# Kernel optimization log

Measured on AMD Instinct MI355X. Metric: run time of the kernel, lower is better.

Reference implementation:

```python
import jax, jax.numpy as jnp
import numpy as np

TEXT_DIM, GIN = 5000, 128
B, N, E = 4096, 200000, 6400000
AE_HID, AE_EMB, G_HID, G_EMB = 8, 4, 8, 4


def _gcn(x, W, b, src, dst):
    N_ = x.shape[0]
    h = x @ W
    loop = jnp.arange(N_)
    s = jnp.concatenate([src, loop])
    d = jnp.concatenate([dst, loop])
    deg = jax.ops.segment_sum(jnp.ones(s.shape[0], h.dtype), d, num_segments=N_)
    dinv = jnp.where(deg > 0, jax.lax.rsqrt(jnp.maximum(deg, 1e-12)), 0.0)
    norm = dinv[s] * dinv[d]
    out = jax.ops.segment_sum(h[s] * norm[:, None], d, num_segments=N_)
    return out + b


def setup_inputs() -> dict:
    key = jax.random.key(0)
    ks = jax.random.split(key, 20)
    def lin(k, fan_in, fan_out):
        lim = 1.0 / np.sqrt(fan_in)
        kw, kb = jax.random.split(k)
        W = jax.random.uniform(kw, (fan_in, fan_out), jnp.float32, -lim, lim)
        b = jax.random.uniform(kb, (fan_out,), jnp.float32, -lim, lim)
        return W, b
    W_e1, b_e1 = lin(ks[0], TEXT_DIM, AE_HID)
    W_e2, b_e2 = lin(ks[1], AE_HID, AE_EMB)
    W_d1, b_d1 = lin(ks[2], AE_EMB, AE_HID)
    W_d2, b_d2 = lin(ks[3], AE_HID, TEXT_DIM)
    W_g1, b_g1 = lin(ks[4], GIN, G_HID)
    W_g2, b_g2 = lin(ks[5], G_HID, G_EMB)
    W_c, b_c = lin(ks[6], AE_EMB + G_EMB, 1)
    text_x = jax.random.normal(ks[7], (B, TEXT_DIM), jnp.float32)
    node_x = jax.random.normal(ks[8], (N, GIN), jnp.float32)
    edge_index = jax.random.randint(ks[9], (2, E), 0, N, jnp.int64 if jax.config.jax_enable_x64 else jnp.int32)
    batch = jnp.sort(jax.random.randint(ks[10], (N,), 0, B, edge_index.dtype))
    return {"text_x": text_x, "node_x": node_x, "edge_index": edge_index, "batch": batch,
            "W_e1": W_e1, "b_e1": b_e1, "W_e2": W_e2, "b_e2": b_e2,
            "W_d1": W_d1, "b_d1": b_d1, "W_d2": W_d2, "b_d2": b_d2,
            "W_g1": W_g1, "b_g1": b_g1, "W_g2": W_g2, "b_g2": b_g2,
            "W_c": W_c, "b_c": b_c}


def reference(text_x, node_x, edge_index, batch,
              W_e1, b_e1, W_e2, b_e2, W_d1, b_d1, W_d2, b_d2,
              W_g1, b_g1, W_g2, b_g2, W_c, b_c):
    # Autoencoder (eval mode: dropout = identity)
    z_text = jax.nn.relu(jax.nn.relu(text_x @ W_e1 + b_e1) @ W_e2 + b_e2)
    x_hat = jax.nn.sigmoid(jax.nn.relu(z_text @ W_d1 + b_d1) @ W_d2 + b_d2)
    # GNN encoder
    src, dst = edge_index[0], edge_index[1]
    h = jax.nn.relu(_gcn(node_x, W_g1, b_g1, src, dst))
    h = _gcn(h, W_g2, b_g2, src, dst)
    # global mean pool over graphs
    nb = text_x.shape[0]
    sums = jax.ops.segment_sum(h, batch, num_segments=nb)
    cnt = jax.ops.segment_sum(jnp.ones(h.shape[0], h.dtype), batch, num_segments=nb)
    z_graph = sums / jnp.maximum(cnt, 1.0)[:, None]
    z = jnp.concatenate([z_text, z_graph], axis=1)
    logits = z @ W_c + b_c
    return (x_hat, logits, z)
```

## Files before the change

### kernel.cpp

```cpp
#include <hip/hip_runtime.h>

#define BB 4096
#define TD 5000
#define NN 200000
#define EE 6400000
#define NBK 782
#define WS_NEED 40081932ull

__global__ void k_init(const int* __restrict__ e, unsigned int* __restrict__ deg,
                       int* __restrict__ flag) {
    int i = blockIdx.x * 256 + threadIdx.x;
    if (i < NN) deg[i] = 1u;
    if (blockIdx.x == 0) {
        __shared__ int r[256];
        int tid = threadIdx.x;
        int acc = 0;
        for (int k = tid; k < 4096; k += 256) acc |= e[2 * k + 1];
        r[tid] = acc;
        __syncthreads();
        for (int s = 128; s > 0; s >>= 1) {
            if (tid < s) r[tid] |= r[tid + s];
            __syncthreads();
        }
        if (tid == 0) *flag = (r[0] == 0) ? 1 : 0;
    }
}

__device__ void role_rank(int rid, int tid, const int* __restrict__ edge,
                          const int* __restrict__ flag, unsigned int* __restrict__ deg,
                          unsigned int* __restrict__ rnk) {
    int f = *flag;
    int base = rid * 2048 + tid;
    int d[8];
#pragma unroll
    for (int k = 0; k < 8; k++) {
        int e = base + k * 256;
        d[k] = f ? edge[2 * (EE + e)] : edge[EE + e];
    }
    unsigned int rr[8];
#pragma unroll
    for (int k = 0; k < 8; k++) rr[k] = atomicAdd(&deg[d[k]], 1u);
#pragma unroll
    for (int k = 0; k < 8; k++) rnk[base + k * 256] = rr[k];
}

__device__ void role_enc(int row, int tid, const float* __restrict__ text,
                         const float* __restrict__ We1, const float* __restrict__ be1,
                         const float* __restrict__ We2, const float* __restrict__ be2,
                         float* __restrict__ z_text) {
    __shared__ float red[8][256];
    __shared__ float t1[8];
    const float4* xrow = (const float4*)(text + (size_t)row * TD);
    float acc[8];
#pragma unroll
    for (int j = 0; j < 8; j++) acc[j] = 0.f;
    for (int v = tid; v < 1250; v += 256) {
        float4 xv = xrow[v];
        const float4* w = (const float4*)(We1 + (size_t)v * 32);
        float xc[4] = {xv.x, xv.y, xv.z, xv.w};
#pragma unroll
        for (int c = 0; c < 4; c++) {
            float4 wa = w[c * 2], wb = w[c * 2 + 1];
            acc[0] += xc[c] * wa.x; acc[1] += xc[c] * wa.y;
            acc[2] += xc[c] * wa.z; acc[3] += xc[c] * wa.w;
            acc[4] += xc[c] * wb.x; acc[5] += xc[c] * wb.y;
            acc[6] += xc[c] * wb.z; acc[7] += xc[c] * wb.w;
        }
    }
#pragma unroll
    for (int j = 0; j < 8; j++) red[j][tid] = acc[j];
    __syncthreads();
    for (int s = 128; s > 0; s >>= 1) {
        if (tid < s) {
#pragma unroll
            for (int j = 0; j < 8; j++) red[j][tid] += red[j][tid + s];
        }
        __syncthreads();
    }
    if (tid < 8) t1[tid] = fmaxf(red[tid][0] + be1[tid], 0.f);
    __syncthreads();
    if (tid < 4) {
        float z = be2[tid];
#pragma unroll
        for (int k = 0; k < 8; k++) z += t1[k] * We2[k * 4 + tid];
        z_text[row * 4 + tid] = fmaxf(z, 0.f);
    }
}

__device__ void role_mm(int mid, int tid, const float* __restrict__ nodex,
                        const float* __restrict__ Wg1, const float* __restrict__ dinv,
                        float* __restrict__ h0g) {
    __shared__ float W[1024];
    for (int i = tid; i < 1024; i += 256) W[i] = Wg1[i];
    __syncthreads();
    int row = mid * 256 + tid;
    if (row >= NN) return;
    const float4* xr = (const float4*)(nodex + (size_t)row * 128);
    float acc[8];
#pragma unroll
    for (int j = 0; j < 8; j++) acc[j] = 0.f;
#pragma unroll 8
    for (int c = 0; c < 32; c++) {
        float4 v = xr[c];
        const float* wr = &W[c * 32];
#pragma unroll
        for (int j = 0; j < 8; j++)
            acc[j] += v.x * wr[j] + v.y * wr[8 + j] + v.z * wr[16 + j] + v.w * wr[24 + j];
    }
    float di = dinv[row];
    float* o = h0g + (size_t)row * 8;
#pragma unroll
    for (int j = 0; j < 8; j++) o[j] = di * acc[j];
}

__device__ void role_place(int pid, int tid, const int* __restrict__ edge,
                           const int* __restrict__ flag, const unsigned int* __restrict__ indptr,
                           const unsigned int* __restrict__ rnk, int* __restrict__ csr) {
    int f = *flag;
    int base = pid * 1024 + tid;
    int s[4], d[4];
#pragma unroll
    for (int k = 0; k < 4; k++) {
        int e = base + k * 256;
        s[k] = f ? edge[2 * e] : edge[e];
        d[k] = f ? edge[2 * (EE + e)] : edge[EE + e];
    }
    unsigned int rr[4];
#pragma unroll
    for (int k = 0; k < 4; k++) rr[k] = rnk[base + k * 256];
    unsigned int ip[4];
#pragma unroll
    for (int k = 0; k < 4; k++) ip[k] = indptr[d[k]];
#pragma unroll
    for (int k = 0; k < 4; k++) csr[ip[k] + rr[k] - 1u] = s[k];
}

__device__ void role_decode(int row, int tid, const float* __restrict__ zsrc, int zstride,
                            const float* __restrict__ Wd1, const float* __restrict__ bd1,
                            const float* __restrict__ Wd2, const float* __restrict__ bd2,
                            float* __restrict__ xhat) {
    float zz[4];
#pragma unroll
    for (int j = 0; j < 4; j++) zz[j] = zsrc[row * zstride + j];
    float t[8];
#pragma unroll
    for (int k = 0; k < 8; k++) {
        float s = bd1[k];
#pragma unroll
        for (int j = 0; j < 4; j++) s += zz[j] * Wd1[j * 8 + k];
        t[k] = fmaxf(s, 0.f);
    }
    float4* orow = (float4*)(xhat + (size_t)row * TD);
    for (int c4 = tid; c4 < 1250; c4 += 256) {
        float4 s = *(const float4*)(bd2 + c4 * 4);
#pragma unroll
        for (int k = 0; k < 8; k++) {
            float4 w = *(const float4*)(Wd2 + (size_t)k * TD + c4 * 4);
            s.x += t[k] * w.x; s.y += t[k] * w.y;
            s.z += t[k] * w.z; s.w += t[k] * w.w;
        }
        s.x = 1.f / (1.f + expf(-s.x));
        s.y = 1.f / (1.f + expf(-s.y));
        s.z = 1.f / (1.f + expf(-s.z));
        s.w = 1.f / (1.f + expf(-s.w));
        orow[c4] = s;
    }
}

__device__ void role_g1(int gid, int tid, const unsigned int* __restrict__ indptr,
                        const int* __restrict__ csr, const float* __restrict__ h0g,
                        const float* __restrict__ dinv, const float* __restrict__ bg1,
                        const float* __restrict__ Wg2, float* __restrict__ h2g) {
    __shared__ float W[32];
    __shared__ float b1[8];
    __shared__ float h1s[4][8];
    if (tid < 32) W[tid] = Wg2[tid];
    if (tid < 8) b1[tid] = bg1[tid];
    __syncthreads();
    int wid = tid >> 6, lane = tid & 63;
    int i = gid * 4 + wid;
    if (i < NN) {
        int beg = indptr[i], end = indptr[i + 1];
        int f = lane & 7;
        float a = 0.f;
        for (int k = beg + (lane >> 3); k < end; k += 8)
            a += h0g[(size_t)csr[k] * 8 + f];
        a += __shfl_xor(a, 8, 64);
        a += __shfl_xor(a, 16, 64);
        a += __shfl_xor(a, 32, 64);
        if (lane < 8) {
            float di = dinv[i];
            h1s[wid][f] = fmaxf(di * (a + h0g[(size_t)i * 8 + f]) + b1[f], 0.f);
        }
    }
    __syncthreads();
    if (i < NN && lane < 4) {
        float di = dinv[i];
        float s = 0.f;
#pragma unroll
        for (int k = 0; k < 8; k++) s += h1s[wid][k] * W[k * 4 + lane];
        h2g[(size_t)i * 4 + lane] = di * s;
    }
}

__global__ __launch_bounds__(256) void k_fat1(
    const int* __restrict__ edge, const int* __restrict__ flag,
    unsigned int* __restrict__ deg, unsigned int* __restrict__ rnk,
    const float* __restrict__ text,
    const float* __restrict__ We1, const float* __restrict__ be1,
    const float* __restrict__ We2, const float* __restrict__ be2,
    float* __restrict__ z_text)
{
    int bid = blockIdx.x, tid = threadIdx.x;
    if (bid < 6250) {
        if (bid & 1) role_enc(bid >> 1, tid, text, We1, be1, We2, be2, z_text);
        else role_rank(bid >> 1, tid, edge, flag, deg, rnk);
    } else {
        role_enc(3125 + (bid - 6250), tid, text, We1, be1, We2, be2, z_text);
    }
}

__global__ __launch_bounds__(256) void k_fat2(
    const int* __restrict__ edge, const int* __restrict__ flag,
    const unsigned int* __restrict__ indptr, const unsigned int* __restrict__ rnk,
    int* __restrict__ csr, const float* __restrict__ nodex,
    const float* __restrict__ Wg1, const float* __restrict__ dinv,
    float* __restrict__ h0g)
{
    int bid = blockIdx.x, tid = threadIdx.x;
    if (bid < 6250) role_place(bid, tid, edge, flag, indptr, rnk, csr);
    else role_mm(bid - 6250, tid, nodex, Wg1, dinv, h0g);
}

__global__ __launch_bounds__(256) void k_g1(
    const unsigned int* __restrict__ indptr, const int* __restrict__ csr,
    const float* __restrict__ h0g, const float* __restrict__ dinv,
    const float* __restrict__ bg1, const float* __restrict__ Wg2,
    float* __restrict__ h2g)
{
    role_g1(blockIdx.x, threadIdx.x, indptr, csr, h0g, dinv, bg1, Wg2, h2g);
}

__global__ __launch_bounds__(256) void k_g1_ws(
    const unsigned int* __restrict__ indptr, const int* __restrict__ csr,
    const float* __restrict__ h0g, const float* __restrict__ dinv,
    const float* __restrict__ bg1, const float* __restrict__ Wg2,
    float* __restrict__ h2g,
    const float* __restrict__ z_text,
    const float* __restrict__ Wd1, const float* __restrict__ bd1,
    const float* __restrict__ Wd2, const float* __restrict__ bd2,
    float* __restrict__ xhat)
{
    int bid = blockIdx.x, tid = threadIdx.x;
    if (bid < 8192) {
        if (bid & 1) role_decode(bid >> 1, tid, z_text, 4, Wd1, bd1, Wd2, bd2, xhat);
        else role_g1(bid >> 1, tid, indptr, csr, h0g, dinv, bg1, Wg2, h2g);
    } else {
        role_g1(bid - 4096, tid, indptr, csr, h0g, dinv, bg1, Wg2, h2g);
    }
}

__global__ __launch_bounds__(256) void k_dec(
    const float* __restrict__ zsrc,
    const float* __restrict__ Wd1, const float* __restrict__ bd1,
    const float* __restrict__ Wd2, const float* __restrict__ bd2,
    float* __restrict__ xhat)
{
    role_decode(blockIdx.x, threadIdx.x, zsrc, 8, Wd1, bd1, Wd2, bd2, xhat);
}

__global__ void kA_all(const unsigned int* __restrict__ deg, float* __restrict__ dinv,
                       unsigned int* __restrict__ bsum, const int* __restrict__ batch,
                       const int* __restrict__ flag, unsigned int* __restrict__ bnd) {
    __shared__ unsigned int s[256];
    int tid = threadIdx.x;
    int i = blockIdx.x * 256 + tid;
    unsigned int c = 0u;
    if (i < NN) {
        unsigned int u = deg[i];
        dinv[i] = rsqrtf((float)u);
        c = u - 1u;
        int fg = *flag;
        int b = fg ? batch[2 * i] : batch[i];
        int bp = (i == 0) ? -1 : (fg ? batch[2 * (i - 1)] : batch[i - 1]);
        for (int bb = bp + 1; bb <= b; bb++) bnd[bb] = (unsigned int)i;
        if (i == NN - 1)
            for (int bb = b + 1; bb <= BB; bb++) bnd[bb] = (unsigned int)NN;
    }
    s[tid] = c;
    __syncthreads();
    for (int st = 128; st > 0; st >>= 1) {
        if (tid < st) s[tid] += s[tid + st];
        __syncthreads();
    }
    if (tid == 0) bsum[blockIdx.x] = s[0];
}

__global__ void kB_scanblocks(const unsigned int* __restrict__ bsum, unsigned int* __restrict__ bpre,
                              unsigned int* __restrict__ indptr) {
    __shared__ unsigned int s[1024];
    int t = threadIdx.x;
    s[t] = (t < NBK) ? bsum[t] : 0u;
    __syncthreads();
    for (int off = 1; off < 1024; off <<= 1) {
        unsigned int v = (t >= off) ? s[t - off] : 0u;
        __syncthreads();
        s[t] += v;
        __syncthreads();
    }
    if (t < NBK) bpre[t] = (t == 0) ? 0u : s[t - 1];
    if (t == 0) indptr[NN] = EE;
}

__global__ void kC_indptr(const unsigned int* __restrict__ deg, const unsigned int* __restrict__ bpre,
                          unsigned int* __restrict__ indptr) {
    __shared__ unsigned int s[256];
    int tid = threadIdx.x;
    int i = blockIdx.x * 256 + tid;
    unsigned int c = (i < NN) ? (deg[i] - 1u) : 0u;
    s[tid] = c;
    __syncthreads();
    for (int off = 1; off < 256; off <<= 1) {
        unsigned int v = (tid >= off) ? s[tid - off] : 0u;
        __syncthreads();
        s[tid] += v;
        __syncthreads();
    }
    if (i < NN) indptr[i] = bpre[blockIdx.x] + s[tid] - c;
}

__global__ __launch_bounds__(256) void k_gather2(
    const unsigned int* __restrict__ indptr, const int* __restrict__ csr_src,
    const float* __restrict__ h2g, const float* __restrict__ dinv,
    const float* __restrict__ bg2, float* __restrict__ h2f)
{
    __shared__ float b2[4];
    int tid = threadIdx.x;
    if (tid < 4) b2[tid] = bg2[tid];
    __syncthreads();
    int wid = tid >> 6, lane = tid & 63;
    int i = blockIdx.x * 4 + wid;
    if (i >= NN) return;
    int beg = indptr[i], end = indptr[i + 1];
    int f = lane & 3;
    float a = 0.f;
    for (int k = beg + (lane >> 2); k < end; k += 16)
        a += h2g[(size_t)csr_src[k] * 4 + f];
    a += __shfl_xor(a, 4, 64);
    a += __shfl_xor(a, 8, 64);
    a += __shfl_xor(a, 16, 64);
    a += __shfl_xor(a, 32, 64);
    if (lane < 4) {
        float di = dinv[i];
        h2f[(size_t)i * 4 + f] = di * (a + h2g[(size_t)i * 4 + f]) + b2[f];
    }
}

__global__ __launch_bounds__(256) void k_final(
    const float* __restrict__ h2f, const unsigned int* __restrict__ bnd,
    const float* __restrict__ z_text, const float* __restrict__ Wc,
    const float* __restrict__ bc, float* __restrict__ out_logits,
    float* __restrict__ out_z)
{
    __shared__ float red[256][4];
    int g = blockIdx.x, tid = threadIdx.x;
    int lo = bnd[g], hi = bnd[g + 1];
    float a0 = 0.f, a1 = 0.f, a2 = 0.f, a3 = 0.f;
    for (int i = lo + tid; i < hi; i += 256) {
        float4 v = *(const float4*)(h2f + (size_t)i * 4);
        a0 += v.x; a1 += v.y; a2 += v.z; a3 += v.w;
    }
    red[tid][0] = a0; red[tid][1] = a1; red[tid][2] = a2; red[tid][3] = a3;
    __syncthreads();
    for (int s = 128; s > 0; s >>= 1) {
        if (tid < s) {
            red[tid][0] += red[tid + s][0]; red[tid][1] += red[tid + s][1];
            red[tid][2] += red[tid + s][2]; red[tid][3] += red[tid + s][3];
        }
        __syncthreads();
    }
    if (tid == 0) {
        float c = (float)(hi - lo);
        c = fmaxf(c, 1.f);
        float z8[8];
#pragma unroll
        for (int j = 0; j < 4; j++) z8[j] = z_text[g * 4 + j];
#pragma unroll
        for (int j = 0; j < 4; j++) z8[4 + j] = red[0][j] / c;
        float l = bc[0];
#pragma unroll
        for (int k = 0; k < 8; k++) l += z8[k] * Wc[k];
        out_logits[g] = l;
#pragma unroll
        for (int k = 0; k < 8; k++) out_z[g * 8 + k] = z8[k];
    }
}

extern "C" void kernel_launch(void* const* d_in, const int* in_sizes, int n_in,
                              void* d_out, int out_size, void* d_ws, size_t ws_size,
                              hipStream_t stream) {
    const float* text  = (const float*)d_in[0];
    const float* nodex = (const float*)d_in[1];
    const int* edge    = (const int*)d_in[2];
    const int* batch   = (const int*)d_in[3];
    const float* We1 = (const float*)d_in[4];
    const float* be1 = (const float*)d_in[5];
    const float* We2 = (const float*)d_in[6];
    const float* be2 = (const float*)d_in[7];
    const float* Wd1 = (const float*)d_in[8];
    const float* bd1 = (const float*)d_in[9];
    const float* Wd2 = (const float*)d_in[10];
    const float* bd2 = (const float*)d_in[11];
    const float* Wg1 = (const float*)d_in[12];
    const float* bg1 = (const float*)d_in[13];
    const float* Wg2 = (const float*)d_in[14];
    const float* bg2 = (const float*)d_in[15];
    const float* Wc  = (const float*)d_in[16];
    const float* bc  = (const float*)d_in[17];

    float* out_xhat   = (float*)d_out;
    float* out_logits = out_xhat + (size_t)BB * TD;
    float* out_z      = out_logits + BB;

    const bool use_ws = (ws_size >= WS_NEED);

    float *h0g, *h2g, *h2f, *dinv, *z_text;
    unsigned int *deg, *indptr, *rnk, *bsum, *bpre, *bnd;
    int *csr, *flag;

    if (use_ws) {
        char* w = (char*)d_ws;
        h0g    = (float*)(w + 0);
        h2g    = (float*)(w + 6400000);
        h2f    = (float*)(w + 9600000);
        dinv   = (float*)(w + 12800000);
        indptr = (unsigned int*)(w + 13600000);
        csr    = (int*)(w + 14400004);
        z_text = (float*)(w + 40000004);
        bnd    = (unsigned int*)(w + 40065540);
        flag   = (int*)(w + 40081928);
        char* o = (char*)d_out;
        rnk  = (unsigned int*)(o + 0);
        deg  = (unsigned int*)(o + 25600000);
        bsum = (unsigned int*)(o + 26400000);
        bpre = (unsigned int*)(o + 26403128);
    } else {
        char* o = (char*)d_out;
        h0g    = (float*)(o + 0);
        h2g    = (float*)(o + 6400000);
        h2f    = (float*)(o + 9600000);
        dinv   = (float*)(o + 12800000);
        deg    = (unsigned int*)(o + 13600000);
        indptr = (unsigned int*)(o + 14400000);
        rnk    = (unsigned int*)(o + 15200004);
        csr    = (int*)(o + 40800004);
        bsum   = (unsigned int*)(o + 66400004);
        bpre   = (unsigned int*)(o + 66403132);
        z_text = (float*)(o + 66406260);
        bnd    = (unsigned int*)(o + 66471796);
        flag   = (int*)(o + 66488184);
    }

    k_init<<<NBK, 256, 0, stream>>>(edge, deg, flag);
    k_fat1<<<7221, 256, 0, stream>>>(edge, flag, deg, rnk,
                                     text, We1, be1, We2, be2, z_text);
    kA_all<<<NBK, 256, 0, stream>>>(deg, dinv, bsum, batch, flag, bnd);
    kB_scanblocks<<<1, 1024, 0, stream>>>(bsum, bpre, indptr);
    kC_indptr<<<NBK, 256, 0, stream>>>(deg, bpre, indptr);
    k_fat2<<<7032, 256, 0, stream>>>(edge, flag, indptr, rnk, csr,
                                     nodex, Wg1, dinv, h0g);

    if (use_ws) {
        k_g1_ws<<<54096, 256, 0, stream>>>(indptr, csr, h0g, dinv, bg1, Wg2, h2g,
                                           z_text, Wd1, bd1, Wd2, bd2, out_xhat);
    } else {
        k_g1<<<(NN + 3) / 4, 256, 0, stream>>>(indptr, csr, h0g, dinv, bg1, Wg2, h2g);
    }

    k_gather2<<<(NN + 3) / 4, 256, 0, stream>>>(indptr, csr, h2g, dinv, bg2, h2f);
    k_final<<<BB, 256, 0, stream>>>(h2f, bnd, z_text, Wc, bc, out_logits, out_z);

    if (!use_ws) {
        k_dec<<<BB, 256, 0, stream>>>(out_z, Wd1, bd1, Wd2, bd2, out_xhat);
    }
}
```

Baseline: 729.8 us.

## Pack rank with destination, fuse node matmul into degree kernel, shrink workspace

```diff
diff --git a/kernel.cpp b/kernel.cpp
--- a/kernel.cpp
+++ b/kernel.cpp
@@ -5,7 +5,7 @@
 #define NN 200000
 #define EE 6400000
 #define NBK 782
-#define WS_NEED 40081932ull
+#define WS_NEED 36881932ull
 
 __global__ void k_init(const int* __restrict__ e, unsigned int* __restrict__ deg,
                        int* __restrict__ flag) {
@@ -28,7 +28,7 @@
 
 __device__ void role_rank(int rid, int tid, const int* __restrict__ edge,
                           const int* __restrict__ flag, unsigned int* __restrict__ deg,
-                          unsigned int* __restrict__ rnk) {
+                          unsigned int* __restrict__ rnkpack) {
     int f = *flag;
     int base = rid * 2048 + tid;
     int d[8];
@@ -41,7 +41,7 @@
 #pragma unroll
     for (int k = 0; k < 8; k++) rr[k] = atomicAdd(&deg[d[k]], 1u);
 #pragma unroll
-    for (int k = 0; k < 8; k++) rnk[base + k * 256] = rr[k];
+    for (int k = 0; k < 8; k++) rnkpack[base + k * 256] = (rr[k] << 18) | (unsigned int)d[k];
 }
 
 __device__ void role_enc(int row, int tid, const float* __restrict__ text,
@@ -85,54 +85,6 @@
         for (int k = 0; k < 8; k++) z += t1[k] * We2[k * 4 + tid];
         z_text[row * 4 + tid] = fmaxf(z, 0.f);
     }
-}
-
-__device__ void role_mm(int mid, int tid, const float* __restrict__ nodex,
-                        const float* __restrict__ Wg1, const float* __restrict__ dinv,
-                        float* __restrict__ h0g) {
-    __shared__ float W[1024];
-    for (int i = tid; i < 1024; i += 256) W[i] = Wg1[i];
-    __syncthreads();
-    int row = mid * 256 + tid;
-    if (row >= NN) return;
-    const float4* xr = (const float4*)(nodex + (size_t)row * 128);
-    float acc[8];
-#pragma unroll
-    for (int j = 0; j < 8; j++) acc[j] = 0.f;
-#pragma unroll 8
-    for (int c = 0; c < 32; c++) {
-        float4 v = xr[c];
-        const float* wr = &W[c * 32];
-#pragma unroll
-        for (int j = 0; j < 8; j++)
-            acc[j] += v.x * wr[j] + v.y * wr[8 + j] + v.z * wr[16 + j] + v.w * wr[24 + j];
-    }
-    float di = dinv[row];
-    float* o = h0g + (size_t)row * 8;
-#pragma unroll
-    for (int j = 0; j < 8; j++) o[j] = di * acc[j];
-}
-
-__device__ void role_place(int pid, int tid, const int* __restrict__ edge,
-                           const int* __restrict__ flag, const unsigned int* __restrict__ indptr,
-                           const unsigned int* __restrict__ rnk, int* __restrict__ csr) {
-    int f = *flag;
-    int base = pid * 1024 + tid;
-    int s[4], d[4];
-#pragma unroll
-    for (int k = 0; k < 4; k++) {
-        int e = base + k * 256;
-        s[k] = f ? edge[2 * e] : edge[e];
-        d[k] = f ? edge[2 * (EE + e)] : edge[EE + e];
-    }
-    unsigned int rr[4];
-#pragma unroll
-    for (int k = 0; k < 4; k++) rr[k] = rnk[base + k * 256];
-    unsigned int ip[4];
-#pragma unroll
-    for (int k = 0; k < 4; k++) ip[k] = indptr[d[k]];
-#pragma unroll
-    for (int k = 0; k < 4; k++) csr[ip[k] + rr[k] - 1u] = s[k];
 }
 
 __device__ void role_decode(int row, int tid, const float* __restrict__ zsrc, int zstride,
@@ -205,7 +157,7 @@
 
 __global__ __launch_bounds__(256) void k_fat1(
     const int* __restrict__ edge, const int* __restrict__ flag,
-    unsigned int* __restrict__ deg, unsigned int* __restrict__ rnk,
+    unsigned int* __restrict__ deg, unsigned int* __restrict__ rnkpack,
     const float* __restrict__ text,
     const float* __restrict__ We1, const float* __restrict__ be1,
     const float* __restrict__ We2, const float* __restrict__ be2,
@@ -214,22 +166,116 @@
     int bid = blockIdx.x, tid = threadIdx.x;
     if (bid < 6250) {
         if (bid & 1) role_enc(bid >> 1, tid, text, We1, be1, We2, be2, z_text);
-        else role_rank(bid >> 1, tid, edge, flag, deg, rnk);
+        else role_rank(bid >> 1, tid, edge, flag, deg, rnkpack);
     } else {
         role_enc(3125 + (bid - 6250), tid, text, We1, be1, We2, be2, z_text);
     }
 }
 
-__global__ __launch_bounds__(256) void k_fat2(
+__global__ __launch_bounds__(256) void k_kAmm(
+    const unsigned int* __restrict__ deg, const int* __restrict__ batch,
+    const int* __restrict__ flag, const float* __restrict__ nodex,
+    const float* __restrict__ Wg1, float* __restrict__ dinv,
+    unsigned int* __restrict__ bsum, unsigned int* __restrict__ bnd,
+    float* __restrict__ h0g)
+{
+    __shared__ float W[1024];
+    __shared__ unsigned int s[256];
+    int tid = threadIdx.x;
+    for (int i = tid; i < 1024; i += 256) W[i] = Wg1[i];
+    int i = blockIdx.x * 256 + tid;
+    unsigned int c = 0u;
+    float di = 0.f;
+    if (i < NN) {
+        unsigned int u = deg[i];
+        di = rsqrtf((float)u);
+        dinv[i] = di;
+        c = u - 1u;
+        int fg = *flag;
+        int b = fg ? batch[2 * i] : batch[i];
+        int bp = (i == 0) ? -1 : (fg ? batch[2 * (i - 1)] : batch[i - 1]);
+        for (int bb = bp + 1; bb <= b; bb++) bnd[bb] = (unsigned int)i;
+        if (i == NN - 1)
+            for (int bb = b + 1; bb <= BB; bb++) bnd[bb] = (unsigned int)NN;
+    }
+    s[tid] = c;
+    __syncthreads();
+    for (int st = 128; st > 0; st >>= 1) {
+        if (tid < st) s[tid] += s[tid + st];
+        __syncthreads();
+    }
+    if (tid == 0) bsum[blockIdx.x] = s[0];
+    if (i >= NN) return;
+    const float4* xr = (const float4*)(nodex + (size_t)i * 128);
+    float acc[8];
+#pragma unroll
+    for (int j = 0; j < 8; j++) acc[j] = 0.f;
+#pragma unroll 8
+    for (int c2 = 0; c2 < 32; c2++) {
+        float4 v = xr[c2];
+        const float* wr = &W[c2 * 32];
+#pragma unroll
+        for (int j = 0; j < 8; j++)
+            acc[j] += v.x * wr[j] + v.y * wr[8 + j] + v.z * wr[16 + j] + v.w * wr[24 + j];
+    }
+    float* o = h0g + (size_t)i * 8;
+#pragma unroll
+    for (int j = 0; j < 8; j++) o[j] = di * acc[j];
+}
+
+__global__ void kB_scanblocks(const unsigned int* __restrict__ bsum, unsigned int* __restrict__ bpre,
+                              unsigned int* __restrict__ indptr) {
+    __shared__ unsigned int s[1024];
+    int t = threadIdx.x;
+    s[t] = (t < NBK) ? bsum[t] : 0u;
+    __syncthreads();
+    for (int off = 1; off < 1024; off <<= 1) {
+        unsigned int v = (t >= off) ? s[t - off] : 0u;
+        __syncthreads();
+        s[t] += v;
+        __syncthreads();
+    }
+    if (t < NBK) bpre[t] = (t == 0) ? 0u : s[t - 1];
+    if (t == 0) indptr[NN] = EE;
+}
+
+__global__ void kC_indptr(const unsigned int* __restrict__ deg, const unsigned int* __restrict__ bpre,
+                          unsigned int* __restrict__ indptr) {
+    __shared__ unsigned int s[256];
+    int tid = threadIdx.x;
+    int i = blockIdx.x * 256 + tid;
+    unsigned int c = (i < NN) ? (deg[i] - 1u) : 0u;
+    s[tid] = c;
+    __syncthreads();
+    for (int off = 1; off < 256; off <<= 1) {
+        unsigned int v = (tid >= off) ? s[tid - off] : 0u;
+        __syncthreads();
+        s[tid] += v;
+        __syncthreads();
+    }
+    if (i < NN) indptr[i] = bpre[blockIdx.x] + s[tid] - c;
+}
+
+__global__ __launch_bounds__(256) void k_place(
     const int* __restrict__ edge, const int* __restrict__ flag,
-    const unsigned int* __restrict__ indptr, const unsigned int* __restrict__ rnk,
-    int* __restrict__ csr, const float* __restrict__ nodex,
-    const float* __restrict__ Wg1, const float* __restrict__ dinv,
-    float* __restrict__ h0g)
-{
-    int bid = blockIdx.x, tid = threadIdx.x;
-    if (bid < 6250) role_place(bid, tid, edge, flag, indptr, rnk, csr);
-    else role_mm(bid - 6250, tid, nodex, Wg1, dinv, h0g);
+    const unsigned int* __restrict__ indptr, const unsigned int* __restrict__ rnkpack,
+    int* __restrict__ csr)
+{
+    int f = *flag;
+    int base = blockIdx.x * 1024 + threadIdx.x;
+    int s[4];
+    unsigned int p[4];
+#pragma unroll
+    for (int k = 0; k < 4; k++) {
+        int e = base + k * 256;
+        s[k] = f ? edge[2 * e] : edge[e];
+        p[k] = rnkpack[e];
+    }
+    unsigned int ip[4];
+#pragma unroll
+    for (int k = 0; k < 4; k++) ip[k] = indptr[p[k] & 0x3FFFFu];
+#pragma unroll
+    for (int k = 0; k < 4; k++) csr[ip[k] + (p[k] >> 18) - 1u] = s[k];
 }
 
 __global__ __launch_bounds__(256) void k_g1(
@@ -241,7 +287,7 @@
     role_g1(blockIdx.x, threadIdx.x, indptr, csr, h0g, dinv, bg1, Wg2, h2g);
 }
 
-__global__ __launch_bounds__(256) void k_g1_ws(
+__global__ __launch_bounds__(256) void k_g1_dec(
     const unsigned int* __restrict__ indptr, const int* __restrict__ csr,
     const float* __restrict__ h0g, const float* __restrict__ dinv,
     const float* __restrict__ bg1, const float* __restrict__ Wg2,
@@ -267,66 +313,6 @@
     float* __restrict__ xhat)
 {
     role_decode(blockIdx.x, threadIdx.x, zsrc, 8, Wd1, bd1, Wd2, bd2, xhat);
-}
-
-__global__ void kA_all(const unsigned int* __restrict__ deg, float* __restrict__ dinv,
-                       unsigned int* __restrict__ bsum, const int* __restrict__ batch,
-                       const int* __restrict__ flag, unsigned int* __restrict__ bnd) {
-    __shared__ unsigned int s[256];
-    int tid = threadIdx.x;
-    int i = blockIdx.x * 256 + tid;
-    unsigned int c = 0u;
-    if (i < NN) {
-        unsigned int u = deg[i];
-        dinv[i] = rsqrtf((float)u);
-        c = u - 1u;
-        int fg = *flag;
-        int b = fg ? batch[2 * i] : batch[i];
-        int bp = (i == 0) ? -1 : (fg ? batch[2 * (i - 1)] : batch[i - 1]);
-        for (int bb = bp + 1; bb <= b; bb++) bnd[bb] = (unsigned int)i;
-        if (i == NN - 1)
-            for (int bb = b + 1; bb <= BB; bb++) bnd[bb] = (unsigned int)NN;
-    }
-    s[tid] = c;
-    __syncthreads();
-    for (int st = 128; st > 0; st >>= 1) {
-        if (tid < st) s[tid] += s[tid + st];
-        __syncthreads();
-    }
-    if (tid == 0) bsum[blockIdx.x] = s[0];
-}
-
-__global__ void kB_scanblocks(const unsigned int* __restrict__ bsum, unsigned int* __restrict__ bpre,
-                              unsigned int* __restrict__ indptr) {
-    __shared__ unsigned int s[1024];
-    int t = threadIdx.x;
-    s[t] = (t < NBK) ? bsum[t] : 0u;
-    __syncthreads();
-    for (int off = 1; off < 1024; off <<= 1) {
-        unsigned int v = (t >= off) ? s[t - off] : 0u;
-        __syncthreads();
-        s[t] += v;
-        __syncthreads();
-    }
-    if (t < NBK) bpre[t] = (t == 0) ? 0u : s[t - 1];
-    if (t == 0) indptr[NN] = EE;
-}
-
-__global__ void kC_indptr(const unsigned int* __restrict__ deg, const unsigned int* __restrict__ bpre,
-                          unsigned int* __restrict__ indptr) {
-    __shared__ unsigned int s[256];
-    int tid = threadIdx.x;
-    int i = blockIdx.x * 256 + tid;
-    unsigned int c = (i < NN) ? (deg[i] - 1u) : 0u;
-    s[tid] = c;
-    __syncthreads();
-    for (int off = 1; off < 256; off <<= 1) {
-        unsigned int v = (tid >= off) ? s[tid - off] : 0u;
-        __syncthreads();
-        s[tid] += v;
-        __syncthreads();
-    }
-    if (i < NN) indptr[i] = bpre[blockIdx.x] + s[tid] - c;
 }
 
 __global__ __launch_bounds__(256) void k_gather2(
@@ -425,54 +411,54 @@
     const bool use_ws = (ws_size >= WS_NEED);
 
     float *h0g, *h2g, *h2f, *dinv, *z_text;
-    unsigned int *deg, *indptr, *rnk, *bsum, *bpre, *bnd;
+    unsigned int *deg, *indptr, *rnkpack, *bsum, *bpre, *bnd;
     int *csr, *flag;
 
     if (use_ws) {
         char* w = (char*)d_ws;
         h0g    = (float*)(w + 0);
+        h2f    = h0g;
         h2g    = (float*)(w + 6400000);
-        h2f    = (float*)(w + 9600000);
-        dinv   = (float*)(w + 12800000);
-        indptr = (unsigned int*)(w + 13600000);
-        csr    = (int*)(w + 14400004);
-        z_text = (float*)(w + 40000004);
-        bnd    = (unsigned int*)(w + 40065540);
-        flag   = (int*)(w + 40081928);
+        dinv   = (float*)(w + 9600000);
+        indptr = (unsigned int*)(w + 10400000);
+        csr    = (int*)(w + 11200004);
+        z_text = (float*)(w + 36800004);
+        bnd    = (unsigned int*)(w + 36865540);
+        flag   = (int*)(w + 36881928);
         char* o = (char*)d_out;
-        rnk  = (unsigned int*)(o + 0);
-        deg  = (unsigned int*)(o + 25600000);
-        bsum = (unsigned int*)(o + 26400000);
-        bpre = (unsigned int*)(o + 26403128);
+        rnkpack = (unsigned int*)(o + 0);
+        deg     = (unsigned int*)(o + 25600000);
+        bsum    = (unsigned int*)(o + 26400000);
+        bpre    = (unsigned int*)(o + 26403128);
     } else {
         char* o = (char*)d_out;
-        h0g    = (float*)(o + 0);
-        h2g    = (float*)(o + 6400000);
-        h2f    = (float*)(o + 9600000);
-        dinv   = (float*)(o + 12800000);
-        deg    = (unsigned int*)(o + 13600000);
-        indptr = (unsigned int*)(o + 14400000);
-        rnk    = (unsigned int*)(o + 15200004);
-        csr    = (int*)(o + 40800004);
-        bsum   = (unsigned int*)(o + 66400004);
-        bpre   = (unsigned int*)(o + 66403132);
-        z_text = (float*)(o + 66406260);
-        bnd    = (unsigned int*)(o + 66471796);
-        flag   = (int*)(o + 66488184);
+        h0g     = (float*)(o + 0);
+        h2g     = (float*)(o + 6400000);
+        h2f     = (float*)(o + 9600000);
+        dinv    = (float*)(o + 12800000);
+        deg     = (unsigned int*)(o + 13600000);
+        indptr  = (unsigned int*)(o + 14400000);
+        rnkpack = (unsigned int*)(o + 15200004);
+        csr     = (int*)(o + 40800004);
+        bsum    = (unsigned int*)(o + 66400004);
+        bpre    = (unsigned int*)(o + 66403132);
+        z_text  = (float*)(o + 66406260);
+        bnd     = (unsigned int*)(o + 66471796);
+        flag    = (int*)(o + 66488184);
     }
 
     k_init<<<NBK, 256, 0, stream>>>(edge, deg, flag);
-    k_fat1<<<7221, 256, 0, stream>>>(edge, flag, deg, rnk,
+    k_fat1<<<7221, 256, 0, stream>>>(edge, flag, deg, rnkpack,
                                      text, We1, be1, We2, be2, z_text);
-    kA_all<<<NBK, 256, 0, stream>>>(deg, dinv, bsum, batch, flag, bnd);
+    k_kAmm<<<NBK, 256, 0, stream>>>(deg, batch, flag, nodex, Wg1,
+                                    dinv, bsum, bnd, h0g);
     kB_scanblocks<<<1, 1024, 0, stream>>>(bsum, bpre, indptr);
     kC_indptr<<<NBK, 256, 0, stream>>>(deg, bpre, indptr);
-    k_fat2<<<7032, 256, 0, stream>>>(edge, flag, indptr, rnk, csr,
-                                     nodex, Wg1, dinv, h0g);
+    k_place<<<6250, 256, 0, stream>>>(edge, flag, indptr, rnkpack, csr);
 
     if (use_ws) {
-        k_g1_ws<<<54096, 256, 0, stream>>>(indptr, csr, h0g, dinv, bg1, Wg2, h2g,
-                                           z_text, Wd1, bd1, Wd2, bd2, out_xhat);
+        k_g1_dec<<<54096, 256, 0, stream>>>(indptr, csr, h0g, dinv, bg1, Wg2, h2g,
+                                            z_text, Wd1, bd1, Wd2, bd2, out_xhat);
     } else {
         k_g1<<<(NN + 3) / 4, 256, 0, stream>>>(indptr, csr, h0g, dinv, bg1, Wg2, h2g);
     }
```

New measurement: 746.0 us. +2.2%, slower.
